# Performance work log

Hardware: AMD Instinct MI355X
Metric: run time of the kernel (lower is better)

The kernel has to match this reference:

```python
import jax, jax.numpy as jnp
import numpy as np

B, N, T, H = 64, 16, 128, 256  # batch, max_neighbors, time_steps, hidden_dim


def setup_inputs() -> dict:
    key = jax.random.key(0)
    ks = jax.random.split(key, 7)
    inv_h = 1.0 / np.sqrt(H)
    return {
        "node_rnn_output": jax.random.normal(ks[0], (B, T, H), jnp.float32),
        "neigh_rnn_output": jax.random.normal(ks[1], (B, N, T, H), jnp.float32),
        "neighbors_number": N,
        "Wq": jax.random.normal(ks[2], (H, H), jnp.float32) * inv_h,
        "Wk": jax.random.normal(ks[3], (H, H), jnp.float32) * inv_h,
        "Wv": jax.random.normal(ks[4], (H, H), jnp.float32) * inv_h,
        "Wb": jax.random.normal(ks[5], (H, H), jnp.float32) * inv_h,
        "b": jnp.zeros((T,), jnp.float32),
    }


def reference(node_rnn_output, neigh_rnn_output, neighbors_number, Wq, Wk, Wv, Wb, b):
    # key_values: node prepended to neighbors -> [B, N+1, T, H]
    kv = jnp.concatenate((node_rnn_output[:, None], neigh_rnn_output), axis=1)
    # torch nn.Linear: x @ W^T
    q = node_rnn_output @ Wq.T            # [B, T, H] (query is identical across neighbor slots)
    key = kv @ Wk.T                       # [B, N+1, T, H]
    value = kv @ Wv.T                     # [B, N+1, T, H]
    # bilinear score: (q @ Wb) @ key^T + b  (b broadcasts over last axis)
    qW = q @ Wb                           # [B, T, H]
    S = jnp.einsum('bth,bnsh->bnts', qW, key) + b  # [B, N+1, T, T]
    A = jax.nn.softmax(S, axis=-1)        # dropout is identity at eval / drop_prob=0
    outputs = jnp.einsum('bnts,bnsh->bnth', A, value)  # [B, N+1, T, H]
    return outputs, A
```

## Files before the change

### kernel.cpp

```cpp
#include <hip/hip_runtime.h>
#include <cstdio>


typedef __bf16 bf16;
typedef __attribute__((ext_vector_type(8))) __bf16 bf16x8;
typedef __attribute__((ext_vector_type(4))) float floatx4;

#define MFMA_BF16 __builtin_amdgcn_mfma_f32_16x16x32_bf16

__device__ __forceinline__ const float* kv_row_ptr(const float* node, const float* neigh, int bn, int s) {
  int b = bn / 17, nn = bn % 17;
  return (nn == 0) ? node + ((size_t)b * 128 + s) * 256
                   : neigh + (((size_t)b * 16 + (nn - 1)) * 128 + s) * 256;
}

__global__ __launch_bounds__(256) void k_wc(const float* __restrict__ Wq, const float* __restrict__ Wb,
                                            float* __restrict__ Wc) {
  int m = blockIdx.x, h = threadIdx.x;
  float acc = 0.f;
  for (int k = 0; k < 256; ++k) acc = fmaf(Wq[k * 256 + m], Wb[k * 256 + h], acc);
  Wc[m * 256 + h] = acc;
}

__global__ __launch_bounds__(256) void k_we(const float* __restrict__ Wc, const float* __restrict__ Wk,
                                            float* __restrict__ We) {
  int m = blockIdx.x, g = threadIdx.x;
  float acc = 0.f;
  for (int k = 0; k < 256; ++k) acc = fmaf(Wc[m * 256 + k], Wk[k * 256 + g], acc);
  We[m * 256 + g] = acc;
}

__global__ __launch_bounds__(256) void k_qwk(const float* __restrict__ X, const float* __restrict__ W,
                                             float* __restrict__ Y) {
  __shared__ float As[32][64];
  __shared__ float Bs[32][64];
  int tid = threadIdx.x;
  int m0 = blockIdx.x * 64, n0 = blockIdx.y * 64;
  int tx = tid & 15, ty = tid >> 4;
  float acc[4][4] = {};
  int r = tid >> 3, c4 = (tid & 7) * 4;
  int kr = tid >> 4, c4b = (tid & 15) * 4;
  for (int k0 = 0; k0 < 256; k0 += 32) {
#pragma unroll
    for (int p = 0; p < 2; ++p) {
      float4 v = *(const float4*)(X + (size_t)(m0 + r + p * 32) * 256 + k0 + c4);
      As[c4 + 0][r + p * 32] = v.x; As[c4 + 1][r + p * 32] = v.y;
      As[c4 + 2][r + p * 32] = v.z; As[c4 + 3][r + p * 32] = v.w;
    }
#pragma unroll
    for (int p = 0; p < 2; ++p) {
      float4 v = *(const float4*)(W + (size_t)(k0 + kr + p * 16) * 256 + n0 + c4b);
      *(float4*)&Bs[kr + p * 16][c4b] = v;
    }
    __syncthreads();
#pragma unroll 8
    for (int k = 0; k < 32; ++k) {
      float a[4], bb[4];
#pragma unroll
      for (int i = 0; i < 4; ++i) a[i] = As[k][ty * 4 + i];
#pragma unroll
      for (int j = 0; j < 4; ++j) bb[j] = Bs[k][tx * 4 + j];
#pragma unroll
      for (int i = 0; i < 4; ++i)
#pragma unroll
        for (int j = 0; j < 4; ++j) acc[i][j] = fmaf(a[i], bb[j], acc[i][j]);
    }
    __syncthreads();
  }
#pragma unroll
  for (int i = 0; i < 4; ++i) {
    float4 v = make_float4(acc[i][0], acc[i][1], acc[i][2], acc[i][3]);
    *(float4*)(Y + (size_t)(m0 + ty * 4 + i) * 256 + n0 + tx * 4) = v;
  }
}

__global__ __launch_bounds__(256) void k_vgemm(const float* __restrict__ node, const float* __restrict__ neigh,
                                               const float* __restrict__ Wv, bf16* __restrict__ V) {
  __shared__ bf16 As[64][32];
  __shared__ bf16 Bs[64][32];
  int tid = threadIdx.x;
  int m0 = blockIdx.x * 64, n0 = blockIdx.y * 64;
  int wave = tid >> 6, lane = tid & 63, lrow = lane & 15, quad = lane >> 4;
  int bn = m0 >> 7, s0 = m0 & 127;
  const float* src = kv_row_ptr(node, neigh, bn, s0);
  floatx4 acc[4];
#pragma unroll
  for (int nt = 0; nt < 4; ++nt) acc[nt] = (floatx4)0.0f;
  int r = tid >> 3, c4 = (tid & 7) * 4;
  for (int k0 = 0; k0 < 256; k0 += 32) {
#pragma unroll
    for (int p = 0; p < 2; ++p) {
      float4 v = *(const float4*)(src + (size_t)(r + p * 32) * 256 + k0 + c4);
      bf16* d = &As[r + p * 32][c4];
      d[0] = (bf16)v.x; d[1] = (bf16)v.y; d[2] = (bf16)v.z; d[3] = (bf16)v.w;
      float4 w = *(const float4*)(Wv + (size_t)(n0 + r + p * 32) * 256 + k0 + c4);
      bf16* d2 = &Bs[r + p * 32][c4];
      d2[0] = (bf16)w.x; d2[1] = (bf16)w.y; d2[2] = (bf16)w.z; d2[3] = (bf16)w.w;
    }
    __syncthreads();
    bf16x8 af = *(const bf16x8*)&As[wave * 16 + lrow][quad * 8];
#pragma unroll
    for (int nt = 0; nt < 4; ++nt) {
      bf16x8 bfv = *(const bf16x8*)&Bs[nt * 16 + lrow][quad * 8];
      acc[nt] = MFMA_BF16(af, bfv, acc[nt], 0, 0, 0);
    }
    __syncthreads();
  }
#pragma unroll
  for (int nt = 0; nt < 4; ++nt)
#pragma unroll
    for (int rg = 0; rg < 4; ++rg)
      V[(size_t)(m0 + wave * 16 + quad * 4 + rg) * 256 + n0 + nt * 16 + lrow] = (bf16)acc[nt][rg];
}

#define QKS 40
#define ABS 136
__global__ __launch_bounds__(256) void k_fused(const float* __restrict__ qWk, const float* __restrict__ node,
                                               const float* __restrict__ neigh, const float* __restrict__ bvec,
                                               const bf16* __restrict__ V,
                                               float* __restrict__ Aout, float* __restrict__ Out) {
  __shared__ __align__(16) char smem[52224];
  bf16* Qhi = (bf16*)smem;
  bf16* Qlo = (bf16*)(smem + 10240);
  bf16* Khi = (bf16*)(smem + 20480);
  bf16* Klo = (bf16*)(smem + 30720);
  bf16* Ab  = (bf16*)smem;
  bf16* Vt  = (bf16*)(smem + 34816);

  int tid = threadIdx.x;
  int w = tid >> 6, lane = tid & 63, lrow = lane & 15, quad = lane >> 4;
  int bn = blockIdx.x;
  const float* Q = qWk + (size_t)(bn / 17) * 128 * 256;
  const float* K = kv_row_ptr(node, neigh, bn, 0);

  int srow = tid >> 1;
  int skb = (tid & 1) * 16;

  floatx4 acc[2][8];
#pragma unroll
  for (int rt = 0; rt < 2; ++rt)
#pragma unroll
    for (int ct = 0; ct < 8; ++ct) acc[rt][ct] = (floatx4)0.0f;

  for (int k0 = 0; k0 < 256; k0 += 32) {
#pragma unroll
    for (int half = 0; half < 2; ++half) {
      const float* qp = Q + (size_t)srow * 256 + k0 + skb + half * 8;
      const float* kp = K + (size_t)srow * 256 + k0 + skb + half * 8;
      float4 q0 = *(const float4*)qp, q1 = *(const float4*)(qp + 4);
      float4 kk0 = *(const float4*)kp, kk1 = *(const float4*)(kp + 4);
      float qf[8] = {q0.x, q0.y, q0.z, q0.w, q1.x, q1.y, q1.z, q1.w};
      float kf[8] = {kk0.x, kk0.y, kk0.z, kk0.w, kk1.x, kk1.y, kk1.z, kk1.w};
      bf16x8 qh, ql, kh, kl;
#pragma unroll
      for (int u = 0; u < 8; ++u) {
        bf16 h = (bf16)qf[u]; qh[u] = h; ql[u] = (bf16)(qf[u] - (float)h);
        bf16 h2 = (bf16)kf[u]; kh[u] = h2; kl[u] = (bf16)(kf[u] - (float)h2);
      }
      int off = srow * QKS + skb + half * 8;
      *(bf16x8*)&Qhi[off] = qh; *(bf16x8*)&Qlo[off] = ql;
      *(bf16x8*)&Khi[off] = kh; *(bf16x8*)&Klo[off] = kl;
    }
    __syncthreads();
    bf16x8 ah[2], al[2];
#pragma unroll
    for (int rt = 0; rt < 2; ++rt) {
      int off = (w * 32 + rt * 16 + lrow) * QKS + quad * 8;
      ah[rt] = *(const bf16x8*)&Qhi[off];
      al[rt] = *(const bf16x8*)&Qlo[off];
    }
#pragma unroll
    for (int ct = 0; ct < 8; ++ct) {
      int off = (ct * 16 + lrow) * QKS + quad * 8;
      bf16x8 bh = *(const bf16x8*)&Khi[off];
      bf16x8 bl = *(const bf16x8*)&Klo[off];
#pragma unroll
      for (int rt = 0; rt < 2; ++rt) {
        acc[rt][ct] = MFMA_BF16(ah[rt], bh, acc[rt][ct], 0, 0, 0);
        acc[rt][ct] = MFMA_BF16(al[rt], bh, acc[rt][ct], 0, 0, 0);
        acc[rt][ct] = MFMA_BF16(ah[rt], bl, acc[rt][ct], 0, 0, 0);
      }
    }
    __syncthreads();
  }

  float bvv[8];
#pragma unroll
  for (int ct = 0; ct < 8; ++ct) bvv[ct] = bvec[ct * 16 + lrow];
#pragma unroll
  for (int rt = 0; rt < 2; ++rt)
#pragma unroll
    for (int r = 0; r < 4; ++r) {
      float mx = -3.402823466e+38f;
#pragma unroll
      for (int ct = 0; ct < 8; ++ct) {
        float v = acc[rt][ct][r] + bvv[ct];
        acc[rt][ct][r] = v;
        mx = fmaxf(mx, v);
      }
#pragma unroll
      for (int off = 1; off < 16; off <<= 1) mx = fmaxf(mx, __shfl_xor(mx, off, 64));
      float s = 0.f;
#pragma unroll
      for (int ct = 0; ct < 8; ++ct) {
        float e = __expf(acc[rt][ct][r] - mx);
        acc[rt][ct][r] = e;
        s += e;
      }
#pragma unroll
      for (int off = 1; off < 16; off <<= 1) s += __shfl_xor(s, off, 64);
      float inv = 1.f / s;
#pragma unroll
      for (int ct = 0; ct < 8; ++ct) acc[rt][ct][r] *= inv;
    }

  float* Ag = Aout + (size_t)bn * 128 * 128;
#pragma unroll
  for (int rt = 0; rt < 2; ++rt)
#pragma unroll
    for (int r = 0; r < 4; ++r) {
      int row = w * 32 + rt * 16 + quad * 4 + r;
#pragma unroll
      for (int ct = 0; ct < 8; ++ct) {
        int s = ct * 16 + lrow;
        float v = acc[rt][ct][r];
        Ag[(size_t)row * 128 + s] = v;
        Ab[row * ABS + s] = (bf16)v;
      }
    }

  const bf16* Vb = V + (size_t)bn * 128 * 256;
  float* Ob = Out + (size_t)bn * 128 * 256;
  int vs = tid & 127, vh = tid >> 7;
  for (int h0 = 0; h0 < 256; h0 += 64) {
#pragma unroll
    for (int it = 0; it < 4; ++it) {
      int idx8 = it * 2 + vh;
      bf16x8 v = *(const bf16x8*)&Vb[(size_t)vs * 256 + h0 + idx8 * 8];
#pragma unroll
      for (int u = 0; u < 8; ++u) Vt[(idx8 * 8 + u) * ABS + vs] = v[u];
    }
    __syncthreads();
    floatx4 pacc[2][4];
#pragma unroll
    for (int rt = 0; rt < 2; ++rt)
#pragma unroll
      for (int ct = 0; ct < 4; ++ct) pacc[rt][ct] = (floatx4)0.0f;
#pragma unroll
    for (int s0 = 0; s0 < 128; s0 += 32) {
      bf16x8 af[2];
#pragma unroll
      for (int rt = 0; rt < 2; ++rt)
        af[rt] = *(const bf16x8*)&Ab[(w * 32 + rt * 16 + lrow) * ABS + s0 + quad * 8];
#pragma unroll
      for (int ct = 0; ct < 4; ++ct) {
        bf16x8 bv8 = *(const bf16x8*)&Vt[(ct * 16 + lrow) * ABS + s0 + quad * 8];
#pragma unroll
        for (int rt = 0; rt < 2; ++rt)
          pacc[rt][ct] = MFMA_BF16(af[rt], bv8, pacc[rt][ct], 0, 0, 0);
      }
    }
#pragma unroll
    for (int rt = 0; rt < 2; ++rt)
#pragma unroll
      for (int ct = 0; ct < 4; ++ct)
#pragma unroll
        for (int r = 0; r < 4; ++r) {
          int row = w * 32 + rt * 16 + quad * 4 + r;
          Ob[(size_t)row * 256 + h0 + ct * 16 + lrow] = pacc[rt][ct][r];
        }
    __syncthreads();
  }
}

extern "C" void kernel_launch(void* const* d_in, const int* in_sizes, int n_in,
                              void* d_out, int out_size, void* d_ws, size_t ws_size,
                              hipStream_t stream) {
  const float* node  = (const float*)d_in[0];
  const float* neigh = (const float*)d_in[1];
  const float* Wq = (const float*)d_in[3];
  const float* Wk = (const float*)d_in[4];
  const float* Wv = (const float*)d_in[5];
  const float* Wb = (const float*)d_in[6];
  const float* bv = (const float*)d_in[7];

  float* out  = (float*)d_out;
  float* Aout = out + (size_t)64 * 17 * 128 * 256;

  size_t need = (size_t)(65536 + 65536 + 2097152) * 4 + (size_t)35651584 * 2;
  if (ws_size < need) { fprintf(stderr, "ws too small: %zu < %zu\n", ws_size, need); return; }
  float* wsf = (float*)d_ws;
  float* Wc  = wsf;
  float* We  = wsf + 65536;
  float* qWk = wsf + 131072;
  bf16*  V   = (bf16*)(wsf + 131072 + 2097152);

  k_wc<<<256, 256, 0, stream>>>(Wq, Wb, Wc);
  k_we<<<256, 256, 0, stream>>>(Wc, Wk, We);
  k_qwk<<<dim3(128, 4), 256, 0, stream>>>(node, We, qWk);
  k_vgemm<<<dim3(2176, 4), 256, 0, stream>>>(node, neigh, Wv, V);
  k_fused<<<1088, 256, 0, stream>>>(qWk, node, neigh, bv, V, Aout, out);
}
```

Baseline: 527.4 us.

## Produce transposed V directly and read it from global in attention kernel

```diff
diff --git a/kernel.cpp b/kernel.cpp
--- a/kernel.cpp
+++ b/kernel.cpp
@@ -28,6 +28,15 @@
   float acc = 0.f;
   for (int k = 0; k < 256; ++k) acc = fmaf(Wc[m * 256 + k], Wk[k * 256 + g], acc);
   We[m * 256 + g] = acc;
+}
+
+__global__ __launch_bounds__(256) void k_wvb(const float* __restrict__ Wv, bf16* __restrict__ Wvb) {
+  int i = (blockIdx.x * 256 + threadIdx.x) * 4;
+  float4 v = *(const float4*)(Wv + i);
+  bf16 o0 = (bf16)v.x, o1 = (bf16)v.y, o2 = (bf16)v.z, o3 = (bf16)v.w;
+  typedef __attribute__((ext_vector_type(4))) __bf16 bf16x4;
+  bf16x4 o = {o0, o1, o2, o3};
+  *(bf16x4*)(Wvb + i) = o;
 }
 
 __global__ __launch_bounds__(256) void k_qwk(const float* __restrict__ X, const float* __restrict__ W,
@@ -74,58 +83,74 @@
   }
 }
 
-__global__ __launch_bounds__(256) void k_vgemm(const float* __restrict__ node, const float* __restrict__ neigh,
-                                               const float* __restrict__ Wv, bf16* __restrict__ V) {
-  __shared__ bf16 As[64][32];
-  __shared__ bf16 Bs[64][32];
+#define KVS 264
+__global__ __launch_bounds__(256, 4) void k_vt(const float* __restrict__ node, const float* __restrict__ neigh,
+                                               const bf16* __restrict__ Wvb, bf16* __restrict__ Vt) {
+  __shared__ bf16 kvs[64 * KVS];
   int tid = threadIdx.x;
-  int m0 = blockIdx.x * 64, n0 = blockIdx.y * 64;
-  int wave = tid >> 6, lane = tid & 63, lrow = lane & 15, quad = lane >> 4;
-  int bn = m0 >> 7, s0 = m0 & 127;
+  int w = tid >> 6, lane = tid & 63, lrow = lane & 15, quad = lane >> 4;
+  int bn = blockIdx.x >> 1, s0 = (blockIdx.x & 1) * 64;
   const float* src = kv_row_ptr(node, neigh, bn, s0);
-  floatx4 acc[4];
-#pragma unroll
-  for (int nt = 0; nt < 4; ++nt) acc[nt] = (floatx4)0.0f;
-  int r = tid >> 3, c4 = (tid & 7) * 4;
+
+  {
+    int srow = tid >> 2, cseg = (tid & 3) * 64;
+    const float* p = src + (size_t)srow * 256 + cseg;
+#pragma unroll
+    for (int c = 0; c < 8; ++c) {
+      float4 a = *(const float4*)(p + c * 8);
+      float4 b = *(const float4*)(p + c * 8 + 4);
+      bf16x8 o = {(bf16)a.x, (bf16)a.y, (bf16)a.z, (bf16)a.w,
+                  (bf16)b.x, (bf16)b.y, (bf16)b.z, (bf16)b.w};
+      *(bf16x8*)&kvs[srow * KVS + cseg + c * 8] = o;
+    }
+  }
+  __syncthreads();
+
+  floatx4 acc[4][4];
+#pragma unroll
+  for (int rt = 0; rt < 4; ++rt)
+#pragma unroll
+    for (int ct = 0; ct < 4; ++ct) acc[rt][ct] = (floatx4)0.0f;
+
   for (int k0 = 0; k0 < 256; k0 += 32) {
-#pragma unroll
-    for (int p = 0; p < 2; ++p) {
-      float4 v = *(const float4*)(src + (size_t)(r + p * 32) * 256 + k0 + c4);
-      bf16* d = &As[r + p * 32][c4];
-      d[0] = (bf16)v.x; d[1] = (bf16)v.y; d[2] = (bf16)v.z; d[3] = (bf16)v.w;
-      float4 w = *(const float4*)(Wv + (size_t)(n0 + r + p * 32) * 256 + k0 + c4);
-      bf16* d2 = &Bs[r + p * 32][c4];
-      d2[0] = (bf16)w.x; d2[1] = (bf16)w.y; d2[2] = (bf16)w.z; d2[3] = (bf16)w.w;
-    }
-    __syncthreads();
-    bf16x8 af = *(const bf16x8*)&As[wave * 16 + lrow][quad * 8];
-#pragma unroll
-    for (int nt = 0; nt < 4; ++nt) {
-      bf16x8 bfv = *(const bf16x8*)&Bs[nt * 16 + lrow][quad * 8];
-      acc[nt] = MFMA_BF16(af, bfv, acc[nt], 0, 0, 0);
-    }
-    __syncthreads();
-  }
-#pragma unroll
-  for (int nt = 0; nt < 4; ++nt)
-#pragma unroll
-    for (int rg = 0; rg < 4; ++rg)
-      V[(size_t)(m0 + wave * 16 + quad * 4 + rg) * 256 + n0 + nt * 16 + lrow] = (bf16)acc[nt][rg];
-}
-
-#define QKS 40
+    bf16x8 bs[4], at[4];
+#pragma unroll
+    for (int ct = 0; ct < 4; ++ct)
+      bs[ct] = *(const bf16x8*)&kvs[(ct * 16 + lrow) * KVS + k0 + quad * 8];
+#pragma unroll
+    for (int rt = 0; rt < 4; ++rt)
+      at[rt] = *(const bf16x8*)&Wvb[(size_t)(w * 64 + rt * 16 + lrow) * 256 + k0 + quad * 8];
+#pragma unroll
+    for (int rt = 0; rt < 4; ++rt)
+#pragma unroll
+      for (int ct = 0; ct < 4; ++ct)
+        acc[rt][ct] = MFMA_BF16(at[rt], bs[ct], acc[rt][ct], 0, 0, 0);
+  }
+
+  bf16* out = Vt + (size_t)bn * 32768;
+#pragma unroll
+  for (int rt = 0; rt < 4; ++rt)
+#pragma unroll
+    for (int ct = 0; ct < 4; ++ct)
+#pragma unroll
+      for (int rg = 0; rg < 4; ++rg) {
+        int h = w * 64 + rt * 16 + quad * 4 + rg;
+        int s = s0 + ct * 16 + lrow;
+        out[h * 128 + s] = (bf16)acc[rt][ct][rg];
+      }
+}
+
 #define ABS 136
-__global__ __launch_bounds__(256) void k_fused(const float* __restrict__ qWk, const float* __restrict__ node,
-                                               const float* __restrict__ neigh, const float* __restrict__ bvec,
-                                               const bf16* __restrict__ V,
-                                               float* __restrict__ Aout, float* __restrict__ Out) {
-  __shared__ __align__(16) char smem[52224];
+__global__ __launch_bounds__(256, 4) void k_fused(const float* __restrict__ qWk, const float* __restrict__ node,
+                                                  const float* __restrict__ neigh, const float* __restrict__ bvec,
+                                                  const bf16* __restrict__ Vt,
+                                                  float* __restrict__ Aout, float* __restrict__ Out) {
+  __shared__ __align__(16) char smem[34816];
   bf16* Qhi = (bf16*)smem;
-  bf16* Qlo = (bf16*)(smem + 10240);
-  bf16* Khi = (bf16*)(smem + 20480);
-  bf16* Klo = (bf16*)(smem + 30720);
+  bf16* Qlo = (bf16*)(smem + 8192);
+  bf16* Khi = (bf16*)(smem + 16384);
+  bf16* Klo = (bf16*)(smem + 24576);
   bf16* Ab  = (bf16*)smem;
-  bf16* Vt  = (bf16*)(smem + 34816);
 
   int tid = threadIdx.x;
   int w = tid >> 6, lane = tid & 63, lrow = lane & 15, quad = lane >> 4;
@@ -157,7 +182,7 @@
         bf16 h = (bf16)qf[u]; qh[u] = h; ql[u] = (bf16)(qf[u] - (float)h);
         bf16 h2 = (bf16)kf[u]; kh[u] = h2; kl[u] = (bf16)(kf[u] - (float)h2);
       }
-      int off = srow * QKS + skb + half * 8;
+      int off = srow * 32 + skb + half * 8;
       *(bf16x8*)&Qhi[off] = qh; *(bf16x8*)&Qlo[off] = ql;
       *(bf16x8*)&Khi[off] = kh; *(bf16x8*)&Klo[off] = kl;
     }
@@ -165,13 +190,13 @@
     bf16x8 ah[2], al[2];
 #pragma unroll
     for (int rt = 0; rt < 2; ++rt) {
-      int off = (w * 32 + rt * 16 + lrow) * QKS + quad * 8;
+      int off = (w * 32 + rt * 16 + lrow) * 32 + quad * 8;
       ah[rt] = *(const bf16x8*)&Qhi[off];
       al[rt] = *(const bf16x8*)&Qlo[off];
     }
 #pragma unroll
     for (int ct = 0; ct < 8; ++ct) {
-      int off = (ct * 16 + lrow) * QKS + quad * 8;
+      int off = (ct * 16 + lrow) * 32 + quad * 8;
       bf16x8 bh = *(const bf16x8*)&Khi[off];
       bf16x8 bl = *(const bf16x8*)&Klo[off];
 #pragma unroll
@@ -229,32 +254,23 @@
       }
     }
 
-  const bf16* Vb = V + (size_t)bn * 128 * 256;
+  const bf16* Vb = Vt + (size_t)bn * 32768;
   float* Ob = Out + (size_t)bn * 128 * 256;
-  int vs = tid & 127, vh = tid >> 7;
   for (int h0 = 0; h0 < 256; h0 += 64) {
-#pragma unroll
-    for (int it = 0; it < 4; ++it) {
-      int idx8 = it * 2 + vh;
-      bf16x8 v = *(const bf16x8*)&Vb[(size_t)vs * 256 + h0 + idx8 * 8];
-#pragma unroll
-      for (int u = 0; u < 8; ++u) Vt[(idx8 * 8 + u) * ABS + vs] = v[u];
-    }
-    __syncthreads();
     floatx4 pacc[2][4];
 #pragma unroll
     for (int rt = 0; rt < 2; ++rt)
 #pragma unroll
       for (int ct = 0; ct < 4; ++ct) pacc[rt][ct] = (floatx4)0.0f;
 #pragma unroll
-    for (int s0 = 0; s0 < 128; s0 += 32) {
+    for (int sk = 0; sk < 128; sk += 32) {
       bf16x8 af[2];
 #pragma unroll
       for (int rt = 0; rt < 2; ++rt)
-        af[rt] = *(const bf16x8*)&Ab[(w * 32 + rt * 16 + lrow) * ABS + s0 + quad * 8];
+        af[rt] = *(const bf16x8*)&Ab[(w * 32 + rt * 16 + lrow) * ABS + sk + quad * 8];
 #pragma unroll
       for (int ct = 0; ct < 4; ++ct) {
-        bf16x8 bv8 = *(const bf16x8*)&Vt[(ct * 16 + lrow) * ABS + s0 + quad * 8];
+        bf16x8 bv8 = *(const bf16x8*)&Vb[(size_t)(h0 + ct * 16 + lrow) * 128 + sk + quad * 8];
 #pragma unroll
         for (int rt = 0; rt < 2; ++rt)
           pacc[rt][ct] = MFMA_BF16(af[rt], bv8, pacc[rt][ct], 0, 0, 0);
@@ -269,7 +285,6 @@
           int row = w * 32 + rt * 16 + quad * 4 + r;
           Ob[(size_t)row * 256 + h0 + ct * 16 + lrow] = pacc[rt][ct][r];
         }
-    __syncthreads();
   }
 }
 
@@ -287,17 +302,19 @@
   float* out  = (float*)d_out;
   float* Aout = out + (size_t)64 * 17 * 128 * 256;
 
-  size_t need = (size_t)(65536 + 65536 + 2097152) * 4 + (size_t)35651584 * 2;
+  size_t need = (size_t)(65536 + 65536 + 2097152) * 4 + (size_t)65536 * 2 + (size_t)35651584 * 2;
   if (ws_size < need) { fprintf(stderr, "ws too small: %zu < %zu\n", ws_size, need); return; }
   float* wsf = (float*)d_ws;
   float* Wc  = wsf;
   float* We  = wsf + 65536;
   float* qWk = wsf + 131072;
-  bf16*  V   = (bf16*)(wsf + 131072 + 2097152);
+  bf16*  Wvb = (bf16*)(wsf + 131072 + 2097152);
+  bf16*  Vt  = Wvb + 65536;
 
   k_wc<<<256, 256, 0, stream>>>(Wq, Wb, Wc);
+  k_wvb<<<64, 256, 0, stream>>>(Wv, Wvb);
   k_we<<<256, 256, 0, stream>>>(Wc, Wk, We);
   k_qwk<<<dim3(128, 4), 256, 0, stream>>>(node, We, qWk);
-  k_vgemm<<<dim3(2176, 4), 256, 0, stream>>>(node, neigh, Wv, V);
-  k_fused<<<1088, 256, 0, stream>>>(qWk, node, neigh, bv, V, Aout, out);
-}
+  k_vt<<<2176, 256, 0, stream>>>(node, neigh, Wvb, Vt);
+  k_fused<<<1088, 256, 0, stream>>>(qWk, node, neigh, bv, Vt, Aout, out);
+}
```

Result: no change. 529.6 us (+0.4%).
